# Optimization experiments

Hardware: AMD Instinct MI355X
Metric: run time of the kernel (lower is better)

## Reference

```python
import jax, jax.numpy as jnp
import numpy as np

BN_EPS = 1e-5
NN_EPS = 1e-8

def _bn_relu(h, gamma, beta):
    # training-mode BatchNorm1d over (B, L) per channel, biased variance
    mean = jnp.mean(h, axis=(0, 2), keepdims=True)
    var = jnp.mean((h - mean) ** 2, axis=(0, 2), keepdims=True)
    hn = (h - mean) * jax.lax.rsqrt(var + BN_EPS)
    return jax.nn.relu(hn * gamma[None, :, None] + beta[None, :, None])

def setup_inputs() -> dict:
    key = jax.random.key(0)
    ks = jax.random.split(key, 8)
    B, N, M, Cin, Cout = 2, 2048, 8192, 512, 256
    return {
        "x1": jax.random.normal(ks[0], (B, N, Cin), jnp.float32),
        "p1": jax.random.uniform(ks[1], (B, N, 3), jnp.float32),
        "x2": jax.random.normal(ks[2], (B, M, Cout), jnp.float32),
        "p2": jax.random.uniform(ks[3], (B, M, 3), jnp.float32),
        "W_up": jax.random.normal(ks[4], (Cout, Cin), jnp.float32) * (1.0 / np.sqrt(Cin)),
        "gamma_up": jnp.ones((Cout,), jnp.float32),
        "beta_up": jnp.zeros((Cout,), jnp.float32),
        "W_lat": jax.random.normal(ks[5], (Cout, Cout), jnp.float32) * (1.0 / np.sqrt(Cout)),
        "gamma_lat": jnp.ones((Cout,), jnp.float32),
        "beta_lat": jnp.zeros((Cout,), jnp.float32),
    }

def reference(x1, p1, x2, p2, W_up, gamma_up, beta_up, W_lat, gamma_lat, beta_lat):
    B, M, _ = p2.shape
    # up_mlp: 1x1 conv (bias=False) + BN + ReLU -> (B, Cout, N)
    h1 = _bn_relu(jnp.einsum('bnc,oc->bon', x1, W_up), gamma_up, beta_up)
    # three_nn: squared distances from each p2 query to all p1 points
    d2 = (jnp.sum(p2 ** 2, -1)[:, :, None] + jnp.sum(p1 ** 2, -1)[:, None, :]
          - 2.0 * jnp.einsum('bmd,bnd->bmn', p2, p1))  # (B, M, N)
    neg_d, idx = jax.lax.top_k(-d2, 3)                 # 3 smallest squared dists
    dist = -neg_d                                      # (B, M, 3)
    dist_recip = 1.0 / (dist + NN_EPS)
    weight = dist_recip / jnp.sum(dist_recip, axis=2, keepdims=True)  # (B, M, 3)
    # three_interpolate: weighted gather of h1 along point axis
    C = h1.shape[1]
    g = jnp.take_along_axis(h1, idx.reshape(B, 1, M * 3), axis=2).reshape(B, C, M, 3)
    interp = jnp.einsum('bcmk,bmk->bcm', g, weight)    # (B, Cout, M)
    # lateral_mlp on x2
    h2 = _bn_relu(jnp.einsum('bmc,oc->bom', x2, W_lat), gamma_lat, beta_lat)
    y = interp + h2                                    # (B, Cout, M)
    return jnp.transpose(y, (0, 2, 1)), p2             # (B, M, Cout), (B, M, 3)
```

## Files before the change

kernel.cpp:

```cpp
#include <hip/hip_runtime.h>

#define BATCH 2
#define NPTS  2048
#define MPTS  8192
#define CIN1  512
#define CIN2  256
#define COUT  256
#define ROWS1 (BATCH*NPTS)
#define ROWS2 (BATCH*MPTS)
#define BN_EPS 1e-5f
#define NN_EPS 1e-8f

#define NCHUNK 16
#define CHUNK  (NPTS / NCHUNK)
#define HCHUNK (CHUNK / 2)

typedef __attribute__((ext_vector_type(8))) short  bf16x8;
typedef __attribute__((ext_vector_type(4))) float  f32x4;

#define AS1 __attribute__((address_space(1)))
#define AS3 __attribute__((address_space(3)))

__device__ __forceinline__ unsigned short bf16_rne(float x) {
    unsigned u = __float_as_uint(x);
    u += 0x7FFFu + ((u >> 16) & 1u);
    return (unsigned short)(u >> 16);
}
__device__ __forceinline__ void gload16(const void* g, void* l) {
    __builtin_amdgcn_global_load_lds((const AS1 unsigned int*)g,
                                     (AS3 unsigned int*)l, 16, 0, 0);
}

__global__ __launch_bounds__(256)
void prep_fused(const float* __restrict__ x1, const float* __restrict__ x2,
                const float* __restrict__ wu, const float* __restrict__ wl,
                const float* __restrict__ p1, const float* __restrict__ p2,
                unsigned short* __restrict__ x1h, unsigned short* __restrict__ x2h,
                unsigned short* __restrict__ wuh, unsigned short* __restrict__ wlh,
                float2* __restrict__ part, float* __restrict__ stats) {
    const int bid = blockIdx.x;
    const int t = threadIdx.x;
    if (bid < 3168) {
        const float* src; unsigned short* dh; int K, tile;
        if (bid < 1024)      { src = x1; dh = x1h; K = CIN1; tile = bid; }
        else if (bid < 3072) { src = x2; dh = x2h; K = CIN2; tile = bid - 1024; }
        else if (bid < 3136) { src = wu; dh = wuh; K = CIN1; tile = bid - 3072; }
        else                 { src = wl; dh = wlh; K = CIN2; tile = bid - 3136; }
        const int ktiles = K / 32;
        const int rt = tile / ktiles, kt = tile - rt * ktiles;
        const int row = t >> 2, lg = t & 3;
        const float* s = src + (size_t)(rt * 64 + row) * K + kt * 32 + lg * 8;
        const float4 v0 = *(const float4*)s;
        const float4 v1 = *(const float4*)(s + 4);
        const float vv[8] = {v0.x, v0.y, v0.z, v0.w, v1.x, v1.y, v1.z, v1.w};
        bf16x8 h;
        #pragma unroll
        for (int i = 0; i < 8; ++i) h[i] = (short)bf16_rne(vv[i]);
        const unsigned off = ((unsigned)(row * 64 + lg * 16)) ^ ((unsigned)((row & 7) << 4));
        *(bf16x8*)((char*)dh + (size_t)tile * 4096 + off) = h;
    } else if (bid < 4192) {
        __shared__ float4 pts[CHUNK];
        const int q = bid - 3168;
        const int b = q >> 9;
        const int r = q & 511;
        const int ck = r >> 5;
        const int mblk = r & 31;
        const int n0 = ck * CHUNK;
        if (t < CHUNK) {
            const float* P1 = p1 + ((size_t)b * NPTS + n0) * 3;
            float x = P1[t * 3 + 0], y = P1[t * 3 + 1], z = P1[t * 3 + 2];
            pts[t] = make_float4(x, y, z, x * x + y * y + z * z);
        }
        __syncthreads();
        const int m = mblk * 256 + t;
        const int row = b * MPTS + m;
        const float* qp = p2 + (size_t)row * 3;
        const float qx = qp[0], qy = qp[1], qz = qp[2];
        const float s2 = qx * qx + qy * qy + qz * qz;
        float dA0 = 1e30f, dA1 = 1e30f, dA2 = 1e30f;
        int   iA0 = 0,     iA1 = 0,     iA2 = 0;
        float dB0 = 1e30f, dB1 = 1e30f, dB2 = 1e30f;
        int   iB0 = 0,     iB1 = 0,     iB2 = 0;
        #pragma unroll 4
        for (int n = 0; n < HCHUNK; ++n) {
            float4 pA = pts[n];
            float4 pB = pts[n + HCHUNK];
            float dA = s2 + pA.w - 2.0f * (pA.x * qx + pA.y * qy + pA.z * qz);
            float dB = s2 + pB.w - 2.0f * (pB.x * qx + pB.y * qy + pB.z * qz);
            if (dA < dA2) {
                if (dA < dA1) {
                    dA2 = dA1; iA2 = iA1;
                    if (dA < dA0) { dA1 = dA0; iA1 = iA0; dA0 = dA; iA0 = n0 + n; }
                    else          { dA1 = dA; iA1 = n0 + n; }
                } else { dA2 = dA; iA2 = n0 + n; }
            }
            if (dB < dB2) {
                if (dB < dB1) {
                    dB2 = dB1; iB2 = iB1;
                    if (dB < dB0) { dB1 = dB0; iB1 = iB0; dB0 = dB; iB0 = n0 + HCHUNK + n; }
                    else          { dB1 = dB; iB1 = n0 + HCHUNK + n; }
                } else { dB2 = dB; iB2 = n0 + HCHUNK + n; }
            }
        }
        #define INS3(d, i) \
            if ((d) < dA2) { \
                if ((d) < dA1) { \
                    dA2 = dA1; iA2 = iA1; \
                    if ((d) < dA0) { dA1 = dA0; iA1 = iA0; dA0 = (d); iA0 = (i); } \
                    else           { dA1 = (d); iA1 = (i); } \
                } else { dA2 = (d); iA2 = (i); } \
            }
        INS3(dB0, iB0); INS3(dB1, iB1); INS3(dB2, iB2);
        #undef INS3
        float2* o = part + ((size_t)ck * ROWS2 + row) * 3;
        o[0] = make_float2(dA0, __int_as_float(iA0));
        o[1] = make_float2(dA1, __int_as_float(iA1));
        o[2] = make_float2(dA2, __int_as_float(iA2));
    } else {
        ((float4*)stats)[t] = (float4){0.f, 0.f, 0.f, 0.f};
    }
}

union GemmLds {
    unsigned char stage[3][2][4096];
    float Ct[64][68];
};

template<int KTILES>
__device__ __forceinline__ void gemm_body(
        const unsigned short* __restrict__ A_img, const unsigned short* __restrict__ B_img,
        float* __restrict__ C, float* __restrict__ stats,
        int bx, int by, GemmLds& S, float red[64][8]) {
    const int tid = threadIdx.x;
    const int lane = tid & 63, wid = tid >> 6;
    const int m0 = by * 64, o0 = bx * 64;
    const int wy = wid >> 1, wx = wid & 1;
    const int lr = lane & 15, lg = lane >> 4;

    const int mat = wid >> 1;
    const int half = wid & 1;
    const unsigned short* src = mat ? B_img : A_img;
    const size_t base = ((size_t)(mat ? bx : by) * KTILES) * 2048 + half * 1024;

    f32x4 acc[2][2];
    #pragma unroll
    for (int i = 0; i < 2; ++i)
        #pragma unroll
        for (int j = 0; j < 2; ++j)
            acc[i][j] = (f32x4){0.f, 0.f, 0.f, 0.f};

    auto STAGE = [&](int buf, int tt) {
        const unsigned short* s = src + base + (size_t)tt * 2048;
        char* l = (char*)&S.stage[buf][mat][half * 2048];
        gload16(s + (size_t)lane * 8, l);
        gload16(s + 512 + (size_t)lane * 8, l + 1024);
    };
    auto FOFF = [&](int row) -> int {
        return (row * 64 + lg * 16) ^ ((row & 7) << 4);
    };

    STAGE(0, 0);
    STAGE(1, 1);

    for (int t = 0; t < KTILES; ++t) {
        if (t + 1 < KTILES) asm volatile("s_waitcnt vmcnt(2)" ::: "memory");
        else                asm volatile("s_waitcnt vmcnt(0)" ::: "memory");
        __builtin_amdgcn_s_barrier();
        __builtin_amdgcn_sched_barrier(0);
        if (t + 2 < KTILES) STAGE((t + 2) % 3, t + 2);

        const int cb = t % 3;
        const char* LA = (const char*)&S.stage[cb][0][0];
        const char* LB = (const char*)&S.stage[cb][1][0];

        bf16x8 fa[2], fb[2];
        #pragma unroll
        for (int i = 0; i < 2; ++i)
            fa[i] = *(const bf16x8*)(LA + FOFF(wy * 32 + i * 16 + lr));
        #pragma unroll
        for (int j = 0; j < 2; ++j)
            fb[j] = *(const bf16x8*)(LB + FOFF(wx * 32 + j * 16 + lr));
        #pragma unroll
        for (int i = 0; i < 2; ++i)
            #pragma unroll
            for (int j = 0; j < 2; ++j)
                acc[i][j] = __builtin_amdgcn_mfma_f32_16x16x32_bf16(fa[i], fb[j], acc[i][j], 0, 0, 0);
    }

    __syncthreads();
    #pragma unroll
    for (int i = 0; i < 2; ++i)
        #pragma unroll
        for (int j = 0; j < 2; ++j) {
            const int col = wx * 32 + j * 16 + lr;
            const int rbase = wy * 32 + i * 16 + lg * 4;
            #pragma unroll
            for (int r = 0; r < 4; ++r)
                S.Ct[rbase + r][col] = acc[i][j][r];
        }
    __syncthreads();
    {
        const int cr = tid >> 4;
        const int cc = (tid & 15) * 4;
        #pragma unroll
        for (int q = 0; q < 4; ++q) {
            const int row = cr + q * 16;
            *(float4*)&C[(size_t)(m0 + row) * COUT + o0 + cc] =
                *(const float4*)&S.Ct[row][cc];
        }
    }
    {
        const int col = tid & 63, rq = tid >> 6;
        float s = 0.f, q2 = 0.f;
        #pragma unroll
        for (int r = 0; r < 16; ++r) {
            float v = S.Ct[rq * 16 + r][col];
            s += v;
            q2 = fmaf(v, v, q2);
        }
        red[col][rq] = s;
        red[col][4 + rq] = q2;
    }
    __syncthreads();
    if (tid < 64) {
        float ss = red[tid][0] + red[tid][1] + red[tid][2] + red[tid][3];
        float qq = red[tid][4] + red[tid][5] + red[tid][6] + red[tid][7];
        atomicAdd(&stats[o0 + tid], ss);
        atomicAdd(&stats[COUT + o0 + tid], qq);
    }
}

__global__ __launch_bounds__(256)
void gemm_fused(const unsigned short* __restrict__ x1h, const unsigned short* __restrict__ wuh,
                const unsigned short* __restrict__ x2h, const unsigned short* __restrict__ wlh,
                float* __restrict__ h1, float* __restrict__ out, float* __restrict__ stats) {
    __shared__ GemmLds S;
    __shared__ float red[64][8];
    const int bid = blockIdx.x;
    if (bid < 256) {
        gemm_body<CIN1/32>(x1h, wuh, h1, stats, bid & 3, bid >> 2, S, red);
    } else {
        const int q = bid - 256;
        gemm_body<CIN2/32>(x2h, wlh, out, stats + 512, q & 3, q >> 2, S, red);
    }
}

__global__ __launch_bounds__(256)
void final_combine(const float* __restrict__ h1, const float* __restrict__ stats,
                   const float* __restrict__ g1, const float* __restrict__ b1,
                   const float* __restrict__ g2, const float* __restrict__ b2,
                   const float2* __restrict__ part, float* __restrict__ out) {
    const int t = threadIdx.x;
    const int row = blockIdx.x * 4 + (t >> 6);
    const int c = (t & 63) * 4;
    const int b = row >> 13;

    float d0 = 1e30f, d1 = 1e30f, d2 = 1e30f;
    int   i0 = 0,     i1 = 0,     i2 = 0;
    #pragma unroll
    for (int ck = 0; ck < NCHUNK; ++ck) {
        const float2* pe = part + ((size_t)ck * ROWS2 + row) * 3;
        #pragma unroll
        for (int h = 0; h < 3; ++h) {
            float2 v = pe[h];
            float d = v.x;
            int   i = __float_as_int(v.y);
            if (d < d2) {
                if (d < d1) {
                    d2 = d1; i2 = i1;
                    if (d < d0) { d1 = d0; i1 = i0; d0 = d; i0 = i; }
                    else        { d1 = d;  i1 = i; }
                } else { d2 = d; i2 = i; }
            }
        }
    }
    const float r0 = 1.0f / (d0 + NN_EPS);
    const float r1 = 1.0f / (d1 + NN_EPS);
    const float r2 = 1.0f / (d2 + NN_EPS);
    const float irs = 1.0f / (r0 + r1 + r2);
    const float w0 = r0 * irs, w1 = r1 * irs, w2 = r2 * irs;

    const float4 sum1 = *(const float4*)&stats[c];
    const float4 sq1  = *(const float4*)&stats[COUT + c];
    const float4 sum2 = *(const float4*)&stats[512 + c];
    const float4 sq2  = *(const float4*)&stats[768 + c];
    const float4 gg1  = *(const float4*)&g1[c];
    const float4 bb1  = *(const float4*)&b1[c];
    const float4 gg2  = *(const float4*)&g2[c];
    const float4 bb2  = *(const float4*)&b2[c];

    const float inv1 = 1.0f / (float)ROWS1, inv2 = 1.0f / (float)ROWS2;
    float4 sc1, sh1, sc2, sh2;
    {
        float m, v;
        m = sum1.x*inv1; v = fmaf(-m,m,sq1.x*inv1); sc1.x = gg1.x/sqrtf(v+BN_EPS); sh1.x = fmaf(-m,sc1.x,bb1.x);
        m = sum1.y*inv1; v = fmaf(-m,m,sq1.y*inv1); sc1.y = gg1.y/sqrtf(v+BN_EPS); sh1.y = fmaf(-m,sc1.y,bb1.y);
        m = sum1.z*inv1; v = fmaf(-m,m,sq1.z*inv1); sc1.z = gg1.z/sqrtf(v+BN_EPS); sh1.z = fmaf(-m,sc1.z,bb1.z);
        m = sum1.w*inv1; v = fmaf(-m,m,sq1.w*inv1); sc1.w = gg1.w/sqrtf(v+BN_EPS); sh1.w = fmaf(-m,sc1.w,bb1.w);
        m = sum2.x*inv2; v = fmaf(-m,m,sq2.x*inv2); sc2.x = gg2.x/sqrtf(v+BN_EPS); sh2.x = fmaf(-m,sc2.x,bb2.x);
        m = sum2.y*inv2; v = fmaf(-m,m,sq2.y*inv2); sc2.y = gg2.y/sqrtf(v+BN_EPS); sh2.y = fmaf(-m,sc2.y,bb2.y);
        m = sum2.z*inv2; v = fmaf(-m,m,sq2.z*inv2); sc2.z = gg2.z/sqrtf(v+BN_EPS); sh2.z = fmaf(-m,sc2.z,bb2.z);
        m = sum2.w*inv2; v = fmaf(-m,m,sq2.w*inv2); sc2.w = gg2.w/sqrtf(v+BN_EPS); sh2.w = fmaf(-m,sc2.w,bb2.w);
    }

    const float* hb = h1 + (size_t)b * NPTS * COUT + c;
    const float4 h0 = *(const float4*)(hb + (size_t)i0 * COUT);
    const float4 h4 = *(const float4*)(hb + (size_t)i1 * COUT);
    const float4 h8 = *(const float4*)(hb + (size_t)i2 * COUT);

    const size_t oi = (size_t)row * COUT + c;
    float4 yv = *(const float4*)&out[oi];
    float4 r;
    r.x = fmaxf(fmaf(yv.x, sc2.x, sh2.x), 0.f)
        + w0 * fmaxf(fmaf(h0.x, sc1.x, sh1.x), 0.f)
        + w1 * fmaxf(fmaf(h4.x, sc1.x, sh1.x), 0.f)
        + w2 * fmaxf(fmaf(h8.x, sc1.x, sh1.x), 0.f);
    r.y = fmaxf(fmaf(yv.y, sc2.y, sh2.y), 0.f)
        + w0 * fmaxf(fmaf(h0.y, sc1.y, sh1.y), 0.f)
        + w1 * fmaxf(fmaf(h4.y, sc1.y, sh1.y), 0.f)
        + w2 * fmaxf(fmaf(h8.y, sc1.y, sh1.y), 0.f);
    r.z = fmaxf(fmaf(yv.z, sc2.z, sh2.z), 0.f)
        + w0 * fmaxf(fmaf(h0.z, sc1.z, sh1.z), 0.f)
        + w1 * fmaxf(fmaf(h4.z, sc1.z, sh1.z), 0.f)
        + w2 * fmaxf(fmaf(h8.z, sc1.z, sh1.z), 0.f);
    r.w = fmaxf(fmaf(yv.w, sc2.w, sh2.w), 0.f)
        + w0 * fmaxf(fmaf(h0.w, sc1.w, sh1.w), 0.f)
        + w1 * fmaxf(fmaf(h4.w, sc1.w, sh1.w), 0.f)
        + w2 * fmaxf(fmaf(h8.w, sc1.w, sh1.w), 0.f);
    *(float4*)&out[oi] = r;
}

extern "C" void kernel_launch(void* const* d_in, const int* in_sizes, int n_in,
                              void* d_out, int out_size, void* d_ws, size_t ws_size,
                              hipStream_t stream) {
    const float* x1       = (const float*)d_in[0];
    const float* p1       = (const float*)d_in[1];
    const float* x2       = (const float*)d_in[2];
    const float* p2       = (const float*)d_in[3];
    const float* W_up     = (const float*)d_in[4];
    const float* gamma_up = (const float*)d_in[5];
    const float* beta_up  = (const float*)d_in[6];
    const float* W_lat    = (const float*)d_in[7];
    const float* gamma_lat= (const float*)d_in[8];
    const float* beta_lat = (const float*)d_in[9];
    float* out = (float*)d_out;

    char* w = (char*)d_ws;
    unsigned short* x1h = (unsigned short*)(w);
    unsigned short* x2h = (unsigned short*)(w + (4u<<20));
    unsigned short* wuh = (unsigned short*)(w + (12u<<20));
    unsigned short* wlh = (unsigned short*)(w + (12u<<20) + (256u<<10));
    float*  h1    = (float*)(w + (13u<<20));
    float*  stats = (float*)(w + (17u<<20));
    float2* part  = (float2*)(w + (17u<<20) + (16u<<10));

    prep_fused<<<4193, 256, 0, stream>>>(x1, x2, W_up, W_lat, p1, p2,
                                         x1h, x2h, wuh, wlh, part, stats);

    gemm_fused<<<1280, 256, 0, stream>>>(x1h, wuh, x2h, wlh, h1, out, stats);

    final_combine<<<ROWS2 / 4, 256, 0, stream>>>(h1, stats, gamma_up, beta_up,
                                                 gamma_lat, beta_lat, part, out);

    hipMemcpyAsync(out + (size_t)ROWS2 * COUT, p2,
                   (size_t)ROWS2 * 3 * sizeof(float),
                   hipMemcpyDeviceToDevice, stream);
}
```

Baseline: 178.3 us.

## Split fused prep kernel into separate convert, nearest-neighbor and memset launches

```diff
diff --git a/kernel.cpp b/kernel.cpp
--- a/kernel.cpp
+++ b/kernel.cpp
@@ -13,7 +13,6 @@
 
 #define NCHUNK 16
 #define CHUNK  (NPTS / NCHUNK)
-#define HCHUNK (CHUNK / 2)
 
 typedef __attribute__((ext_vector_type(8))) short  bf16x8;
 typedef __attribute__((ext_vector_type(4))) float  f32x4;
@@ -32,93 +31,80 @@
 }
 
 __global__ __launch_bounds__(256)
-void prep_fused(const float* __restrict__ x1, const float* __restrict__ x2,
-                const float* __restrict__ wu, const float* __restrict__ wl,
-                const float* __restrict__ p1, const float* __restrict__ p2,
-                unsigned short* __restrict__ x1h, unsigned short* __restrict__ x2h,
-                unsigned short* __restrict__ wuh, unsigned short* __restrict__ wlh,
-                float2* __restrict__ part, float* __restrict__ stats) {
+void split_pre(const float* __restrict__ x1, const float* __restrict__ x2,
+               const float* __restrict__ wu, const float* __restrict__ wl,
+               unsigned short* __restrict__ x1h, unsigned short* __restrict__ x2h,
+               unsigned short* __restrict__ wuh, unsigned short* __restrict__ wlh) {
     const int bid = blockIdx.x;
     const int t = threadIdx.x;
-    if (bid < 3168) {
-        const float* src; unsigned short* dh; int K, tile;
-        if (bid < 1024)      { src = x1; dh = x1h; K = CIN1; tile = bid; }
-        else if (bid < 3072) { src = x2; dh = x2h; K = CIN2; tile = bid - 1024; }
-        else if (bid < 3136) { src = wu; dh = wuh; K = CIN1; tile = bid - 3072; }
-        else                 { src = wl; dh = wlh; K = CIN2; tile = bid - 3136; }
-        const int ktiles = K / 32;
-        const int rt = tile / ktiles, kt = tile - rt * ktiles;
-        const int row = t >> 2, lg = t & 3;
-        const float* s = src + (size_t)(rt * 64 + row) * K + kt * 32 + lg * 8;
-        const float4 v0 = *(const float4*)s;
-        const float4 v1 = *(const float4*)(s + 4);
-        const float vv[8] = {v0.x, v0.y, v0.z, v0.w, v1.x, v1.y, v1.z, v1.w};
-        bf16x8 h;
-        #pragma unroll
-        for (int i = 0; i < 8; ++i) h[i] = (short)bf16_rne(vv[i]);
-        const unsigned off = ((unsigned)(row * 64 + lg * 16)) ^ ((unsigned)((row & 7) << 4));
-        *(bf16x8*)((char*)dh + (size_t)tile * 4096 + off) = h;
-    } else if (bid < 4192) {
-        __shared__ float4 pts[CHUNK];
-        const int q = bid - 3168;
-        const int b = q >> 9;
-        const int r = q & 511;
-        const int ck = r >> 5;
-        const int mblk = r & 31;
-        const int n0 = ck * CHUNK;
-        if (t < CHUNK) {
-            const float* P1 = p1 + ((size_t)b * NPTS + n0) * 3;
-            float x = P1[t * 3 + 0], y = P1[t * 3 + 1], z = P1[t * 3 + 2];
-            pts[t] = make_float4(x, y, z, x * x + y * y + z * z);
-        }
-        __syncthreads();
-        const int m = mblk * 256 + t;
-        const int row = b * MPTS + m;
-        const float* qp = p2 + (size_t)row * 3;
-        const float qx = qp[0], qy = qp[1], qz = qp[2];
-        const float s2 = qx * qx + qy * qy + qz * qz;
-        float dA0 = 1e30f, dA1 = 1e30f, dA2 = 1e30f;
-        int   iA0 = 0,     iA1 = 0,     iA2 = 0;
-        float dB0 = 1e30f, dB1 = 1e30f, dB2 = 1e30f;
-        int   iB0 = 0,     iB1 = 0,     iB2 = 0;
-        #pragma unroll 4
-        for (int n = 0; n < HCHUNK; ++n) {
-            float4 pA = pts[n];
-            float4 pB = pts[n + HCHUNK];
-            float dA = s2 + pA.w - 2.0f * (pA.x * qx + pA.y * qy + pA.z * qz);
-            float dB = s2 + pB.w - 2.0f * (pB.x * qx + pB.y * qy + pB.z * qz);
-            if (dA < dA2) {
-                if (dA < dA1) {
-                    dA2 = dA1; iA2 = iA1;
-                    if (dA < dA0) { dA1 = dA0; iA1 = iA0; dA0 = dA; iA0 = n0 + n; }
-                    else          { dA1 = dA; iA1 = n0 + n; }
-                } else { dA2 = dA; iA2 = n0 + n; }
-            }
-            if (dB < dB2) {
-                if (dB < dB1) {
-                    dB2 = dB1; iB2 = iB1;
-                    if (dB < dB0) { dB1 = dB0; iB1 = iB0; dB0 = dB; iB0 = n0 + HCHUNK + n; }
-                    else          { dB1 = dB; iB1 = n0 + HCHUNK + n; }
-                } else { dB2 = dB; iB2 = n0 + HCHUNK + n; }
-            }
-        }
-        #define INS3(d, i) \
-            if ((d) < dA2) { \
-                if ((d) < dA1) { \
-                    dA2 = dA1; iA2 = iA1; \
-                    if ((d) < dA0) { dA1 = dA0; iA1 = iA0; dA0 = (d); iA0 = (i); } \
-                    else           { dA1 = (d); iA1 = (i); } \
-                } else { dA2 = (d); iA2 = (i); } \
-            }
-        INS3(dB0, iB0); INS3(dB1, iB1); INS3(dB2, iB2);
-        #undef INS3
-        float2* o = part + ((size_t)ck * ROWS2 + row) * 3;
-        o[0] = make_float2(dA0, __int_as_float(iA0));
-        o[1] = make_float2(dA1, __int_as_float(iA1));
-        o[2] = make_float2(dA2, __int_as_float(iA2));
-    } else {
-        ((float4*)stats)[t] = (float4){0.f, 0.f, 0.f, 0.f};
-    }
+    const float* src; unsigned short* dh; int K, tile;
+    if (bid < 1024)      { src = x1; dh = x1h; K = CIN1; tile = bid; }
+    else if (bid < 3072) { src = x2; dh = x2h; K = CIN2; tile = bid - 1024; }
+    else if (bid < 3136) { src = wu; dh = wuh; K = CIN1; tile = bid - 3072; }
+    else                 { src = wl; dh = wlh; K = CIN2; tile = bid - 3136; }
+    const int ktiles = K / 32;
+    const int rt = tile / ktiles, kt = tile - rt * ktiles;
+    const int row = t >> 2, lg = t & 3;
+    const float* s = src + (size_t)(rt * 64 + row) * K + kt * 32 + lg * 8;
+    const float4 v0 = *(const float4*)s;
+    const float4 v1 = *(const float4*)(s + 4);
+    const float vv[8] = {v0.x, v0.y, v0.z, v0.w, v1.x, v1.y, v1.z, v1.w};
+    bf16x8 h;
+    #pragma unroll
+    for (int i = 0; i < 8; ++i) h[i] = (short)bf16_rne(vv[i]);
+    const unsigned off = ((unsigned)(row * 64 + lg * 16)) ^ ((unsigned)((row & 7) << 4));
+    *(bf16x8*)((char*)dh + (size_t)tile * 4096 + off) = h;
+}
+
+__global__ __launch_bounds__(256)
+void nn_part(const float* __restrict__ p1, const float* __restrict__ p2,
+             float2* __restrict__ part) {
+    __shared__ float4 pts[CHUNK];
+    const int b = blockIdx.z;
+    const int ck = blockIdx.y;
+    const int mblk = blockIdx.x;
+    const int t = threadIdx.x;
+    const int n0 = ck * CHUNK;
+    if (t < CHUNK) {
+        const float* P1 = p1 + ((size_t)b * NPTS + n0) * 3;
+        float x = P1[t * 3 + 0], y = P1[t * 3 + 1], z = P1[t * 3 + 2];
+        pts[t] = make_float4(x, y, z, x * x + y * y + z * z);
+    }
+    __syncthreads();
+    const int m = mblk * 256 + t;
+    const int row = b * MPTS + m;
+    const float* qp = p2 + (size_t)row * 3;
+    const float qx = qp[0], qy = qp[1], qz = qp[2];
+    const float s2 = qx * qx + qy * qy + qz * qz;
+    float d0 = 1e30f, d1 = 1e30f, d2 = 1e30f;
+    int   i0 = 0,     i1 = 0,     i2 = 0;
+    #define INS(d, i) \
+        if ((d) < d2) { \
+            if ((d) < d1) { \
+                d2 = d1; i2 = i1; \
+                if ((d) < d0) { d1 = d0; i1 = i0; d0 = (d); i0 = (i); } \
+                else          { d1 = (d); i1 = (i); } \
+            } else { d2 = (d); i2 = (i); } \
+        }
+    for (int n = 0; n < CHUNK; n += 4) {
+        float4 pa = pts[n + 0];
+        float4 pb = pts[n + 1];
+        float4 pc = pts[n + 2];
+        float4 pd = pts[n + 3];
+        float da = s2 + pa.w - 2.0f * (pa.x * qx + pa.y * qy + pa.z * qz);
+        float db = s2 + pb.w - 2.0f * (pb.x * qx + pb.y * qy + pb.z * qz);
+        float dc = s2 + pc.w - 2.0f * (pc.x * qx + pc.y * qy + pc.z * qz);
+        float dd = s2 + pd.w - 2.0f * (pd.x * qx + pd.y * qy + pd.z * qz);
+        INS(da, n0 + n + 0);
+        INS(db, n0 + n + 1);
+        INS(dc, n0 + n + 2);
+        INS(dd, n0 + n + 3);
+    }
+    #undef INS
+    float2* o = part + ((size_t)ck * ROWS2 + row) * 3;
+    o[0] = make_float2(d0, __int_as_float(i0));
+    o[1] = make_float2(d1, __int_as_float(i1));
+    o[2] = make_float2(d2, __int_as_float(i2));
 }
 
 union GemmLds {
@@ -354,8 +340,11 @@
     float*  stats = (float*)(w + (17u<<20));
     float2* part  = (float2*)(w + (17u<<20) + (16u<<10));
 
-    prep_fused<<<4193, 256, 0, stream>>>(x1, x2, W_up, W_lat, p1, p2,
-                                         x1h, x2h, wuh, wlh, part, stats);
+    hipMemsetAsync(stats, 0, 1024 * sizeof(float), stream);
+
+    split_pre<<<3168, 256, 0, stream>>>(x1, x2, W_up, W_lat, x1h, x2h, wuh, wlh);
+
+    nn_part<<<dim3(MPTS / 256, NCHUNK, BATCH), 256, 0, stream>>>(p1, p2, part);
 
     gemm_fused<<<1280, 256, 0, stream>>>(x1h, wuh, x2h, wlh, h1, out, stats);
 
```

After: 175.0 us. Within noise of the previous version (-1.8%).
